# Performance work log

Measured on AMD Instinct MI355X. Metric: run time of the kernel, lower is better.

Reference implementation:

```python
import jax, jax.numpy as jnp
import numpy as np

DECAY = 0.999
EPS = 1e-05


def setup_inputs() -> dict:
    key = jax.random.key(0)
    k1, k2 = jax.random.split(key)
    B, L, S, D, E = 32, 8, 512, 256, 2048
    x = jax.random.normal(k1, (B, L, S, D), dtype=jnp.float32)
    # stacked per-quantizer codebooks: embed[l] is the [dim, n_embed] buffer of Quantize l
    embed = jax.random.normal(k2, (L, D, E), dtype=jnp.float32)
    cluster_size = jnp.zeros((L, E), dtype=jnp.float32)
    embed_avg = embed.copy()
    return {"x": x, "embed": embed, "cluster_size": cluster_size, "embed_avg": embed_avg}


def reference(x, embed, cluster_size, embed_avg):
    # x: [B, L, S, D]; embed: [L, D, E]; cluster_size: [L, E]; embed_avg: [L, D, E]
    B, L, S, D = x.shape
    E = embed.shape[-1]

    dist = ((x * x).sum(-1, keepdims=True)
            - 2.0 * jnp.einsum('blsd,lde->blse', x, embed)
            + (embed * embed).sum(1)[None, :, None, :])
    ids = jnp.argmin(dist, axis=-1)  # argmax of -dist == argmin of dist; [B, L, S]

    # codebook lookup: embed_t[l, ids[b,l,s]] -> [B, L, S, D]
    embed_t = jnp.swapaxes(embed, 1, 2)  # [L, E, D]
    q = embed_t[jnp.arange(L)[None, :, None], ids]

    # EMA buffer updates (training mode; done on .data in torch, i.e. no grad)
    l_idx = jnp.broadcast_to(jnp.arange(L)[None, :, None], (B, L, S))
    counts = jnp.zeros((L, E), x.dtype).at[l_idx, ids].add(1.0)  # onehot.sum(0) per quantizer
    embed_sum = jnp.zeros((L, E, D), x.dtype).at[l_idx, ids].add(jax.lax.stop_gradient(x))
    embed_sum = jnp.swapaxes(embed_sum, 1, 2)  # [L, D, E] == flatten.T @ onehot
    new_cluster_size = DECAY * cluster_size + (1.0 - DECAY) * counts
    new_embed_avg = DECAY * embed_avg + (1.0 - DECAY) * embed_sum
    n = new_cluster_size.sum(-1, keepdims=True)  # [L, 1]
    cs = (new_cluster_size + EPS) / (n + E * EPS) * n
    new_embed = new_embed_avg / cs[:, None, :]

    # NOTE: the original loop overwrites `diff` each iteration then does `diff += diff`,
    # so the returned diff is 2 * diff_of_last_quantizer / length (faithfully reproduced).
    diff_last = jnp.mean((jax.lax.stop_gradient(q[:, L - 1]) - x[:, L - 1]) ** 2)
    diff = 2.0 * diff_last / L

    # straight-through estimator
    out = x + jax.lax.stop_gradient(q - x)
    return out, diff, ids, new_embed, new_cluster_size, new_embed_avg
```

## Files before the change

### kernel.cpp

```cpp
#include <hip/hip_runtime.h>

#define LL 8
#define BB 32
#define SS 512
#define DD 256
#define EE 2048
#define LED (LL*DD*EE)
#define LE  (LL*EE)
#define NROWS (BB*LL*SS)
#define NSEG 32

typedef __bf16 bf16x8 __attribute__((ext_vector_type(8)));
typedef float  f32x16 __attribute__((ext_vector_type(16)));

__global__ void transpose_norms_kernel(const float* __restrict__ embed,
                                       float* __restrict__ embed_t,
                                       float* __restrict__ norms) {
    __shared__ float tile[32][33];
    const int l  = blockIdx.z;
    const int d0 = blockIdx.y * 32;
    const int e0 = blockIdx.x * 32;
    const int tx = threadIdx.x, ty = threadIdx.y;

    float v = embed[((size_t)l*DD + d0 + ty)*EE + e0 + tx];
    tile[ty][tx] = v;
    __syncthreads();
    embed_t[((size_t)l*EE + e0 + ty)*DD + d0 + tx] = tile[tx][ty];
    __syncthreads();
    tile[ty][tx] = v * v;
    __syncthreads();
    if (ty == 0) {
        float s = 0.f;
        #pragma unroll
        for (int i = 0; i < 32; ++i) s += tile[i][tx];
        atomicAdd(&norms[l*EE + e0 + tx], s);
    }
}

__global__ void prep_embed_frag(const float* __restrict__ embed,
                                __bf16* __restrict__ frag) {
    const int bid  = blockIdx.x;
    const int s    = bid & 31;
    const int m    = (bid >> 5) & 63;
    const int l    = bid >> 11;
    const int lane = threadIdx.x;
    const int e    = m*32 + (lane & 31);
    const int ks   = ((s >> 4) << 3) + ((s & 15) >> 1);
    const bool lo  = s & 1;
    const int kbase = ks*16 + (lane >> 5)*8;

    bf16x8 v;
    #pragma unroll
    for (int j = 0; j < 8; ++j) {
        float val = embed[((size_t)l*DD + kbase + j)*EE + e];
        __bf16 h = (__bf16)val;
        v[j] = lo ? (__bf16)(val - (float)h) : h;
    }
    *(bf16x8*)(frag + (size_t)bid*512 + lane*8) = v;
}

__global__ __launch_bounds__(256, 3)
void argmin_mfma(const float* __restrict__ x,
                 const __bf16* __restrict__ frag,
                 const float* __restrict__ embed_t,
                 const float* __restrict__ norms,
                 int* __restrict__ ids_out,
                 int* __restrict__ counts_i,
                 float* __restrict__ out,
                 float* __restrict__ diff_acc) {
    __shared__ __bf16 slots[2][16*512];
    __shared__ float  normbuf[EE];

    const int tid  = threadIdx.x;
    const int wave = tid >> 6, lane = tid & 63;
    const int l    = blockIdx.x & 7;
    const int rb   = blockIdx.x >> 3;
    const int idx  = rb*4 + wave;
    const int b    = idx >> 4, st = idx & 15;
    const int rowtile = (b*LL + l)*16 + st;

    {
        const float* np = norms + l*EE;
        for (int i = wave; i < 8; i += 4) {
            __builtin_amdgcn_global_load_lds(
                (const __attribute__((address_space(1))) void*)(np + i*256 + lane*4),
                (__attribute__((address_space(3))) void*)(normbuf + i*256), 16, 0, 0);
        }
    }

    bf16x8 bh[16], bl[16];
    {
        const float* xr = x + (size_t)(rowtile*32 + (lane & 31))*DD + (lane >> 5)*8;
        #pragma unroll
        for (int ks = 0; ks < 16; ++ks) {
            float4 v0 = *(const float4*)(xr + ks*16);
            float4 v1 = *(const float4*)(xr + ks*16 + 4);
            float f[8] = {v0.x, v0.y, v0.z, v0.w, v1.x, v1.y, v1.z, v1.w};
            #pragma unroll
            for (int j = 0; j < 8; ++j) {
                __bf16 h = (__bf16)f[j];
                bh[ks][j] = h;
                bl[ks][j] = (__bf16)(f[j] - (float)h);
            }
        }
    }

    const __bf16* fl = frag + (size_t)l*64*NSEG*512;

    auto stage_half = [&](int m, int half, int slot) {
        const __bf16* src = fl + ((size_t)m*NSEG + half*16)*512 + lane*8;
        __bf16* dst = &slots[slot][0];
        for (int i = wave; i < 16; i += 4) {
            __builtin_amdgcn_global_load_lds(
                (const __attribute__((address_space(1))) void*)(src + i*512),
                (__attribute__((address_space(3))) void*)(dst + i*512), 16, 0, 0);
        }
    };

    float maxv = -3.4e38f;
    int   maxi = 0;

    stage_half(0, 0, 0);
    __syncthreads();

    #pragma unroll 1
    for (int t = 0; t < 64; ++t) {
        stage_half(t, 1, 1);

        f32x16 acc;
        #pragma unroll
        for (int i = 0; i < 16; ++i) acc[i] = 0.0f;

        #pragma unroll
        for (int k = 0; k < 8; ++k) {
            bf16x8 ah = *(const bf16x8*)(&slots[0][0] + (2*k    )*512 + lane*8);
            bf16x8 al = *(const bf16x8*)(&slots[0][0] + (2*k + 1)*512 + lane*8);
            acc = __builtin_amdgcn_mfma_f32_32x32x16_bf16(ah, bh[k], acc, 0, 0, 0);
            acc = __builtin_amdgcn_mfma_f32_32x32x16_bf16(ah, bl[k], acc, 0, 0, 0);
            acc = __builtin_amdgcn_mfma_f32_32x32x16_bf16(al, bh[k], acc, 0, 0, 0);
        }
        __syncthreads();

        if (t < 63) stage_half(t + 1, 0, 0);

        #pragma unroll
        for (int k = 0; k < 8; ++k) {
            bf16x8 ah = *(const bf16x8*)(&slots[1][0] + (2*k    )*512 + lane*8);
            bf16x8 al = *(const bf16x8*)(&slots[1][0] + (2*k + 1)*512 + lane*8);
            acc = __builtin_amdgcn_mfma_f32_32x32x16_bf16(ah, bh[8+k], acc, 0, 0, 0);
            acc = __builtin_amdgcn_mfma_f32_32x32x16_bf16(ah, bl[8+k], acc, 0, 0, 0);
            acc = __builtin_amdgcn_mfma_f32_32x32x16_bf16(al, bh[8+k], acc, 0, 0, 0);
        }

        const int ebase = t*32 + 4*(lane >> 5);
        #pragma unroll
        for (int j = 0; j < 4; ++j) {
            float4 nv = *(const float4*)(normbuf + t*32 + 8*j + 4*(lane >> 5));
            #pragma unroll
            for (int rr = 0; rr < 4; ++rr) {
                float v = fmaf(-0.5f, (&nv.x)[rr], acc[4*j + rr]);
                int e = ebase + rr + 8*j;
                if (v > maxv) { maxv = v; maxi = e; }
            }
        }
        __syncthreads();
    }

    float ov = __shfl_xor(maxv, 32, 64);
    int   oi = __shfl_xor(maxi, 32, 64);
    if (ov > maxv || (ov == maxv && oi < maxi)) { maxv = ov; maxi = oi; }
    if (lane < 32) {
        ids_out[(size_t)rowtile*32 + lane] = maxi;
        atomicAdd(&counts_i[l*EE + maxi], 1);
    }

    const float4* et4  = (const float4*)embed_t;
    const float4* x4   = (const float4*)x;
    float4*       out4 = (float4*)out;
    float sq = 0.f;
    #pragma unroll 4
    for (int r = 0; r < 32; ++r) {
        int id = __shfl(maxi, r);
        float4 qv = et4[((size_t)l*EE + id)*64 + lane];
        size_t o = ((size_t)rowtile*32 + r)*64 + lane;
        out4[o] = qv;
        if (l == LL - 1) {
            float4 xv = x4[o];
            float dx = qv.x - xv.x, dy = qv.y - xv.y, dz = qv.z - xv.z, dw = qv.w - xv.w;
            sq += dx*dx + dy*dy + dz*dz + dw*dw;
        }
    }
    if (l == LL - 1) {
        #pragma unroll
        for (int off = 32; off; off >>= 1) sq += __shfl_down(sq, off);
        if (lane == 0) atomicAdd(diff_acc, sq);
    }
}

__global__ __launch_bounds__(256)
void scan_kernel(const int* __restrict__ counts_i,
                 const float* __restrict__ cs_in,
                 int* __restrict__ bin_start,
                 int* __restrict__ cursor,
                 float* __restrict__ ncs_out,
                 float* __restrict__ n_out) {
    __shared__ int part[256];
    __shared__ float red[4];
    const int l = blockIdx.x, tid = threadIdx.x;
    const int base = l*EE + tid*8;
    int local[8], tsum = 0;
    float fsum = 0.f;
    #pragma unroll
    for (int j = 0; j < 8; ++j) {
        local[j] = counts_i[base + j];
        tsum += local[j];
        float v = 0.999f*cs_in[base + j] + 0.001f*(float)local[j];
        ncs_out[base + j] = v;
        fsum += v;
    }
    part[tid] = tsum;
    __syncthreads();
    for (int off = 1; off < 256; off <<= 1) {
        int v = (tid >= off) ? part[tid - off] : 0;
        __syncthreads();
        part[tid] += v;
        __syncthreads();
    }
    int run = part[tid] - tsum;
    #pragma unroll
    for (int j = 0; j < 8; ++j) {
        bin_start[base + j] = run;
        cursor[base + j]    = run;
        run += local[j];
    }
    #pragma unroll
    for (int off = 32; off; off >>= 1) fsum += __shfl_down(fsum, off);
    if ((tid & 63) == 0) red[tid >> 6] = fsum;
    __syncthreads();
    if (tid == 0) n_out[l] = red[0] + red[1] + red[2] + red[3];
}

__global__ __launch_bounds__(256)
void scatter_idx_kernel(const int* __restrict__ ids,
                        int* __restrict__ cursor,
                        int* __restrict__ sorted_rows) {
    const int r = blockIdx.x*256 + threadIdx.x;
    const int l = (r >> 9) & 7;
    const int e = ids[r];
    int pos = atomicAdd(&cursor[l*EE + e], 1);
    sorted_rows[l*(NROWS/LL) + pos] = r;
}

__global__ __launch_bounds__(256)
void segsum_kernel(const float* __restrict__ x,
                   const int* __restrict__ sorted_rows,
                   const int* __restrict__ bin_start,
                   const int* __restrict__ counts_i,
                   float* __restrict__ embed_sum) {
    const int bid = blockIdx.x;
    const int l   = bid >> 11;
    const int e   = bid & 2047;
    const int tid = threadIdx.x;
    const int start = bin_start[l*EE + e];
    const int cnt   = counts_i[l*EE + e];
    const int* rows = sorted_rows + l*(NROWS/LL);

    float acc = 0.f;
    int i = 0;
    for (; i + 1 < cnt; i += 2) {
        int r0 = rows[start + i], r1 = rows[start + i + 1];
        acc += x[(size_t)r0*DD + tid] + x[(size_t)r1*DD + tid];
    }
    if (i < cnt) acc += x[(size_t)rows[start + i]*DD + tid];
    embed_sum[((size_t)l*EE + e)*DD + tid] = acc;
}

__global__ void finalize_embed_kernel(const float* __restrict__ embed_avg,
                                      const float* __restrict__ embed_sum,
                                      const float* __restrict__ ncs,
                                      const float* __restrict__ n,
                                      float* __restrict__ nea_out,
                                      float* __restrict__ ne_out) {
    __shared__ float tile[32][33];
    const int l  = blockIdx.z;
    const int d0 = blockIdx.y * 32;
    const int e0 = blockIdx.x * 32;
    const int tx = threadIdx.x, ty = threadIdx.y;

    tile[ty][tx] = embed_sum[((size_t)l*EE + e0 + ty)*DD + d0 + tx];
    __syncthreads();
    const size_t idx = ((size_t)l*DD + d0 + ty)*EE + e0 + tx;
    float nea = 0.999f*embed_avg[idx] + 0.001f*tile[tx][ty];
    nea_out[idx] = nea;
    float nl = n[l];
    float c  = ncs[l*EE + e0 + tx];
    float cs = (c + 1e-5f) / (nl + 0.02048f) * nl;
    ne_out[idx] = nea / cs;
}

__global__ void diff_scale_kernel(const float* __restrict__ diff_acc,
                                  float* __restrict__ diff_out) {
    *diff_out = (*diff_acc / (float)(BB*SS*DD)) * 0.25f;
}

extern "C" void kernel_launch(void* const* d_in, const int* in_sizes, int n_in,
                              void* d_out, int out_size, void* d_ws, size_t ws_size,
                              hipStream_t stream) {
    const float* x            = (const float*)d_in[0];
    const float* embed        = (const float*)d_in[1];
    const float* cluster_size = (const float*)d_in[2];
    const float* embed_avg    = (const float*)d_in[3];

    float* out      = (float*)d_out;
    float* diff_out = out + 33554432;
    int*   ids_out  = (int*)(out + 33554433);
    float* ne_out   = out + 33685505;
    float* ncs_out  = out + 37879809;
    float* nea_out  = out + 37896193;

    float* ws        = (float*)d_ws;
    float* embed_t   = ws;
    float* embed_sum = ws + LED;
    int*   counts_i  = (int*)(ws + 2*(size_t)LED);
    float* norms     = ws + 2*(size_t)LED + LE;
    float* diff_acc  = norms + LE;
    float* n_ws      = diff_acc + 1;
    int*   bin_start = (int*)(n_ws + LL);
    int*   cursor    = bin_start + LE;
    int*   sorted_rows = cursor + LE;
    __bf16* embfrag  = (__bf16*)(sorted_rows + NROWS + 16);

    hipMemsetAsync(counts_i, 0, (size_t)(2*LE + 1) * sizeof(float), stream);

    transpose_norms_kernel<<<dim3(EE/32, DD/32, LL), dim3(32, 32), 0, stream>>>(
        embed, embed_t, norms);

    prep_embed_frag<<<LL*64*NSEG, 64, 0, stream>>>(embed, embfrag);

    argmin_mfma<<<1024, 256, 0, stream>>>(x, embfrag, embed_t, norms, ids_out,
                                          counts_i, out, diff_acc);

    scan_kernel<<<LL, 256, 0, stream>>>(counts_i, cluster_size, bin_start, cursor,
                                        ncs_out, n_ws);

    scatter_idx_kernel<<<NROWS/256, 256, 0, stream>>>(ids_out, cursor, sorted_rows);

    segsum_kernel<<<LE, 256, 0, stream>>>(x, sorted_rows, bin_start, counts_i, embed_sum);

    finalize_embed_kernel<<<dim3(EE/32, DD/32, LL), dim3(32, 32), 0, stream>>>(
        embed_avg, embed_sum, ncs_out, n_ws, nea_out, ne_out);

    diff_scale_kernel<<<1, 1, 0, stream>>>(diff_acc, diff_out);
}
```

Baseline: 1.009 ms.

## Fuse embed prep kernels and restructure argmin MFMA loop with full-tile double buffering

Merges the bf16 hi/lo fragment preparation into the transpose/norm kernel, so embed is read once and one launch goes away. In argmin, each codebook tile (all 32 segments) is now double-buffered in LDS with a single sync per tile instead of half-tile staging with two syncs. The three MFMA chains go into separate accumulators to break the serial dependence, and s_setprio is raised around the MFMA block. LDS use doubles and occupancy is lowered to 2 blocks per CU. The extra accumulators also change the order of the fp32 sums slightly.

```diff
diff --git a/kernel.cpp b/kernel.cpp
--- a/kernel.cpp
+++ b/kernel.cpp
@@ -13,9 +13,10 @@
 typedef __bf16 bf16x8 __attribute__((ext_vector_type(8)));
 typedef float  f32x16 __attribute__((ext_vector_type(16)));
 
-__global__ void transpose_norms_kernel(const float* __restrict__ embed,
-                                       float* __restrict__ embed_t,
-                                       float* __restrict__ norms) {
+__global__ void prep_transpose_kernel(const float* __restrict__ embed,
+                                      float* __restrict__ embed_t,
+                                      float* __restrict__ norms,
+                                      __bf16* __restrict__ frag) {
     __shared__ float tile[32][33];
     const int l  = blockIdx.z;
     const int d0 = blockIdx.y * 32;
@@ -25,41 +26,32 @@
     float v = embed[((size_t)l*DD + d0 + ty)*EE + e0 + tx];
     tile[ty][tx] = v;
     __syncthreads();
+
     embed_t[((size_t)l*EE + e0 + ty)*DD + d0 + tx] = tile[tx][ty];
-    __syncthreads();
-    tile[ty][tx] = v * v;
-    __syncthreads();
+
+    const int t    = ty*32 + tx;
+    const int ksl  = t >> 9;
+    const int pos  = t & 511;
+    const int lane = pos >> 3, j = pos & 7;
+    const int klocal = (lane >> 5)*8 + j;
+    const int e_loc  = lane & 31;
+    float val = tile[ksl*16 + klocal][e_loc];
+    __bf16 h = (__bf16)val;
+    const int m  = blockIdx.x;
+    const int ks = (d0 >> 4) + ksl;
+    size_t segbase = (((size_t)(l*64 + m))*NSEG + 2*ks)*512 + pos;
+    frag[segbase]       = h;
+    frag[segbase + 512] = (__bf16)(val - (float)h);
+
     if (ty == 0) {
         float s = 0.f;
         #pragma unroll
-        for (int i = 0; i < 32; ++i) s += tile[i][tx];
+        for (int i = 0; i < 32; ++i) s += tile[i][tx]*tile[i][tx];
         atomicAdd(&norms[l*EE + e0 + tx], s);
     }
 }
 
-__global__ void prep_embed_frag(const float* __restrict__ embed,
-                                __bf16* __restrict__ frag) {
-    const int bid  = blockIdx.x;
-    const int s    = bid & 31;
-    const int m    = (bid >> 5) & 63;
-    const int l    = bid >> 11;
-    const int lane = threadIdx.x;
-    const int e    = m*32 + (lane & 31);
-    const int ks   = ((s >> 4) << 3) + ((s & 15) >> 1);
-    const bool lo  = s & 1;
-    const int kbase = ks*16 + (lane >> 5)*8;
-
-    bf16x8 v;
-    #pragma unroll
-    for (int j = 0; j < 8; ++j) {
-        float val = embed[((size_t)l*DD + kbase + j)*EE + e];
-        __bf16 h = (__bf16)val;
-        v[j] = lo ? (__bf16)(val - (float)h) : h;
-    }
-    *(bf16x8*)(frag + (size_t)bid*512 + lane*8) = v;
-}
-
-__global__ __launch_bounds__(256, 3)
+__global__ __launch_bounds__(256, 2)
 void argmin_mfma(const float* __restrict__ x,
                  const __bf16* __restrict__ frag,
                  const float* __restrict__ embed_t,
@@ -68,7 +60,7 @@
                  int* __restrict__ counts_i,
                  float* __restrict__ out,
                  float* __restrict__ diff_acc) {
-    __shared__ __bf16 slots[2][16*512];
+    __shared__ __bf16 slots[2][NSEG*512];
     __shared__ float  normbuf[EE];
 
     const int tid  = threadIdx.x;
@@ -107,10 +99,10 @@
 
     const __bf16* fl = frag + (size_t)l*64*NSEG*512;
 
-    auto stage_half = [&](int m, int half, int slot) {
-        const __bf16* src = fl + ((size_t)m*NSEG + half*16)*512 + lane*8;
-        __bf16* dst = &slots[slot][0];
-        for (int i = wave; i < 16; i += 4) {
+    auto stage = [&](int m, int buf) {
+        const __bf16* src = fl + (size_t)m*NSEG*512 + lane*8;
+        __bf16* dst = &slots[buf][0];
+        for (int i = wave; i < NSEG; i += 4) {
             __builtin_amdgcn_global_load_lds(
                 (const __attribute__((address_space(1))) void*)(src + i*512),
                 (__attribute__((address_space(3))) void*)(dst + i*512), 16, 0, 0);
@@ -120,45 +112,38 @@
     float maxv = -3.4e38f;
     int   maxi = 0;
 
-    stage_half(0, 0, 0);
+    stage(0, 0);
     __syncthreads();
 
     #pragma unroll 1
-    for (int t = 0; t < 64; ++t) {
-        stage_half(t, 1, 1);
-
-        f32x16 acc;
-        #pragma unroll
-        for (int i = 0; i < 16; ++i) acc[i] = 0.0f;
-
-        #pragma unroll
-        for (int k = 0; k < 8; ++k) {
-            bf16x8 ah = *(const bf16x8*)(&slots[0][0] + (2*k    )*512 + lane*8);
-            bf16x8 al = *(const bf16x8*)(&slots[0][0] + (2*k + 1)*512 + lane*8);
-            acc = __builtin_amdgcn_mfma_f32_32x32x16_bf16(ah, bh[k], acc, 0, 0, 0);
-            acc = __builtin_amdgcn_mfma_f32_32x32x16_bf16(ah, bl[k], acc, 0, 0, 0);
-            acc = __builtin_amdgcn_mfma_f32_32x32x16_bf16(al, bh[k], acc, 0, 0, 0);
-        }
-        __syncthreads();
-
-        if (t < 63) stage_half(t + 1, 0, 0);
-
-        #pragma unroll
-        for (int k = 0; k < 8; ++k) {
-            bf16x8 ah = *(const bf16x8*)(&slots[1][0] + (2*k    )*512 + lane*8);
-            bf16x8 al = *(const bf16x8*)(&slots[1][0] + (2*k + 1)*512 + lane*8);
-            acc = __builtin_amdgcn_mfma_f32_32x32x16_bf16(ah, bh[8+k], acc, 0, 0, 0);
-            acc = __builtin_amdgcn_mfma_f32_32x32x16_bf16(ah, bl[8+k], acc, 0, 0, 0);
-            acc = __builtin_amdgcn_mfma_f32_32x32x16_bf16(al, bh[8+k], acc, 0, 0, 0);
-        }
-
-        const int ebase = t*32 + 4*(lane >> 5);
+    for (int m = 0; m < 64; ++m) {
+        const int buf = m & 1;
+        if (m < 63) stage(m + 1, buf ^ 1);
+
+        f32x16 a0, a1, a2;
+        #pragma unroll
+        for (int i = 0; i < 16; ++i) { a0[i] = 0.0f; a1[i] = 0.0f; a2[i] = 0.0f; }
+
+        const __bf16* sA = &slots[buf][0];
+        __builtin_amdgcn_s_setprio(1);
+        #pragma unroll
+        for (int k = 0; k < 16; ++k) {
+            bf16x8 ah = *(const bf16x8*)(sA + (2*k    )*512 + lane*8);
+            bf16x8 al = *(const bf16x8*)(sA + (2*k + 1)*512 + lane*8);
+            a0 = __builtin_amdgcn_mfma_f32_32x32x16_bf16(ah, bh[k], a0, 0, 0, 0);
+            a1 = __builtin_amdgcn_mfma_f32_32x32x16_bf16(ah, bl[k], a1, 0, 0, 0);
+            a2 = __builtin_amdgcn_mfma_f32_32x32x16_bf16(al, bh[k], a2, 0, 0, 0);
+        }
+        __builtin_amdgcn_s_setprio(0);
+
+        const int ebase = m*32 + 4*(lane >> 5);
         #pragma unroll
         for (int j = 0; j < 4; ++j) {
-            float4 nv = *(const float4*)(normbuf + t*32 + 8*j + 4*(lane >> 5));
+            float4 nv = *(const float4*)(normbuf + m*32 + 8*j + 4*(lane >> 5));
             #pragma unroll
             for (int rr = 0; rr < 4; ++rr) {
-                float v = fmaf(-0.5f, (&nv.x)[rr], acc[4*j + rr]);
+                float v = a0[4*j + rr] + a1[4*j + rr] + a2[4*j + rr];
+                v = fmaf(-0.5f, (&nv.x)[rr], v);
                 int e = ebase + rr + 8*j;
                 if (v > maxv) { maxv = v; maxi = e; }
             }
@@ -332,10 +317,8 @@
 
     hipMemsetAsync(counts_i, 0, (size_t)(2*LE + 1) * sizeof(float), stream);
 
-    transpose_norms_kernel<<<dim3(EE/32, DD/32, LL), dim3(32, 32), 0, stream>>>(
-        embed, embed_t, norms);
-
-    prep_embed_frag<<<LL*64*NSEG, 64, 0, stream>>>(embed, embfrag);
+    prep_transpose_kernel<<<dim3(EE/32, DD/32, LL), dim3(32, 32), 0, stream>>>(
+        embed, embed_t, norms, embfrag);
 
     argmin_mfma<<<1024, 256, 0, stream>>>(x, embfrag, embed_t, norms, ids_out,
                                           counts_i, out, diff_acc);
```

After: 959.7 us. -4.9%, faster.
